# Optimization experiments

Hardware: AMD Instinct MI355X
Metric: run time of the kernel (lower is better)

## Reference

```python
import jax, jax.numpy as jnp
import numpy as np

NUM_EXPERTS = 8
TOP_K = 2
D = 1024


def setup_inputs() -> dict:
    key = jax.random.key(0)
    ks = jax.random.split(key, 5)
    T = 16384
    x = jax.random.normal(ks[0], (T, D), dtype=jnp.float32)
    # torch nn.Linear params: weight [out, in], bias [out]
    Wg = jax.random.normal(ks[1], (NUM_EXPERTS, D), dtype=jnp.float32) * (1.0 / np.sqrt(D))
    bg = jnp.zeros((NUM_EXPERTS,), dtype=jnp.float32)
    We = jax.random.normal(ks[2], (NUM_EXPERTS, D, D), dtype=jnp.float32) * (1.0 / np.sqrt(D))
    be = jax.random.normal(ks[3], (NUM_EXPERTS, D), dtype=jnp.float32) * 0.01
    return {"x": x, "Wg": Wg, "bg": bg, "We": We, "be": be}


def reference(x, Wg, bg, We, be):
    T = x.shape[0]
    # gate logits [T, E]
    gate_logits = x @ Wg.T + bg
    top_k_gates, top_k_idx = jax.lax.top_k(gate_logits, TOP_K)  # [T, K]
    top_k_gates = jax.nn.softmax(top_k_gates, axis=-1)
    # dense per-expert combine weight: sum of gate probs where idx == e
    combine = jnp.zeros((T, NUM_EXPERTS), dtype=x.dtype)
    combine = combine.at[jnp.arange(T)[:, None], top_k_idx].add(top_k_gates)  # [T, E]
    # all-expert dense matmul (faithful to the original naive loop): [E, T, out]
    expert_out = jnp.einsum('td,eod->eto', x, We) + be[:, None, :]
    # weighted combine: output[t] = sum_e combine[t,e] * expert_out[e,t]
    out = jnp.einsum('te,eto->to', combine, expert_out)
    return out
```

## Files before the change

kernel.cpp:

```cpp
#include <hip/hip_runtime.h>
#include <hip/hip_bf16.h>
#include <stdint.h>

#define DDIM 1024
#define NEXP 8
#define SEG  16384

typedef __attribute__((ext_vector_type(8))) short bf16x8;
typedef __attribute__((ext_vector_type(4))) float f32x4;
typedef __attribute__((ext_vector_type(8))) unsigned short u16x8;

__device__ __forceinline__ unsigned short f2bf(float f) {
    union { float f; unsigned int u; } v; v.f = f;
    unsigned int u = v.u;
    return (unsigned short)((u + 0x7FFFu + ((u >> 16) & 1u)) >> 16);
}

__global__ void cvt_we(const float* __restrict__ We, unsigned short* __restrict__ web) {
    size_t idx = ((size_t)blockIdx.x * 256 + threadIdx.x) * 8;
    const float4* p = (const float4*)(We + idx);
    float4 a = p[0], b = p[1];
    u16x8 h;
    h[0] = f2bf(a.x); h[1] = f2bf(a.y); h[2] = f2bf(a.z); h[3] = f2bf(a.w);
    h[4] = f2bf(b.x); h[5] = f2bf(b.y); h[6] = f2bf(b.z); h[7] = f2bf(b.w);
    *(u16x8*)(web + idx) = h;
}

__global__ __launch_bounds__(512) void gate_route(
    const float* __restrict__ x, const float* __restrict__ Wg,
    const float* __restrict__ bg, unsigned short* __restrict__ xb,
    int* __restrict__ cnt, int* __restrict__ tok_list,
    float* __restrict__ gate_list) {

    int wave = threadIdx.x >> 6, lane = threadIdx.x & 63;
    int tbase = blockIdx.x * 32;

    __shared__ int   se[64];
    __shared__ float sg[64];

#pragma unroll
    for (int i = 0; i < 4; i++) {
        int lt = wave * 4 + i;
        int t = tbase + lt;
        const float* xr = x + (size_t)t * DDIM;
        int c0 = lane * 16;

        float4 v[4];
#pragma unroll
        for (int j = 0; j < 4; j++) v[j] = ((const float4*)(xr + c0))[j];

        u16x8 h0, h1;
        h0[0] = f2bf(v[0].x); h0[1] = f2bf(v[0].y); h0[2] = f2bf(v[0].z); h0[3] = f2bf(v[0].w);
        h0[4] = f2bf(v[1].x); h0[5] = f2bf(v[1].y); h0[6] = f2bf(v[1].z); h0[7] = f2bf(v[1].w);
        h1[0] = f2bf(v[2].x); h1[1] = f2bf(v[2].y); h1[2] = f2bf(v[2].z); h1[3] = f2bf(v[2].w);
        h1[4] = f2bf(v[3].x); h1[5] = f2bf(v[3].y); h1[6] = f2bf(v[3].z); h1[7] = f2bf(v[3].w);
        u16x8* xo = (u16x8*)(xb + (size_t)t * DDIM + c0);
        xo[0] = h0; xo[1] = h1;

        float acc[NEXP];
#pragma unroll
        for (int e = 0; e < NEXP; e++) {
            const float4* wg = (const float4*)(Wg + e * DDIM + c0);
            float s = 0.f;
#pragma unroll
            for (int j = 0; j < 4; j++) {
                float4 w = wg[j];
                s += v[j].x * w.x + v[j].y * w.y + v[j].z * w.z + v[j].w * w.w;
            }
            acc[e] = s;
        }
#pragma unroll
        for (int e = 0; e < NEXP; e++) {
#pragma unroll
            for (int o = 32; o > 0; o >>= 1) acc[e] += __shfl_xor(acc[e], o, 64);
        }

        if (lane == 0) {
            float l1 = -1e30f, l2 = -1e30f; int e1 = 0, e2 = 0;
#pragma unroll
            for (int e = 0; e < NEXP; e++) {
                float le = acc[e] + bg[e];
                if (le > l1) { l2 = l1; e2 = e1; l1 = le; e1 = e; }
                else if (le > l2) { l2 = le; e2 = e; }
            }
            float g1 = 1.0f / (1.0f + __expf(l2 - l1));
            float g2 = 1.0f - g1;
            se[lt * 2]     = e1; sg[lt * 2]     = g1;
            se[lt * 2 + 1] = e2; sg[lt * 2 + 1] = g2;
        }
    }
    __syncthreads();

    if (threadIdx.x < NEXP) {
        int e = threadIdx.x;
        int k = 0;
#pragma unroll 8
        for (int i = 0; i < 64; i++) k += (se[i] == e);
        if (k) {
            int p = atomicAdd(cnt + e, k);
            for (int i = 0; i < 64; i++) {
                if (se[i] == e) {
                    tok_list[e * SEG + p]  = (tbase + (i >> 1)) * 2 + (i & 1);
                    gate_list[e * SEG + p] = sg[i];
                    p++;
                }
            }
        }
    }
}

template<bool STORE>
__global__ __launch_bounds__(256, 3) void moe_gemm(
    const unsigned short* __restrict__ xb, const unsigned short* __restrict__ web,
    const float* __restrict__ be, const int* __restrict__ cnt,
    const int* __restrict__ tok_list, const float* __restrict__ gate_list,
    float* __restrict__ dst) {

    int e = blockIdx.y >> 7;
    int m0 = (blockIdx.y & 127) << 7;
    int c = cnt[e];
    if (m0 >= c) return;
    int n0 = blockIdx.x << 7;

    __shared__ unsigned short lA[128 * 64];
    __shared__ unsigned short lB[128 * 64];
    __shared__ int   tok_s[128];
    __shared__ float gate_s[128];

    int tid = threadIdx.x;
    int wave = tid >> 6, lane = tid & 63;

    if (tid < 128) {
        int r = m0 + tid;
        int rc = min(r, c - 1);
        tok_s[tid]  = tok_list[e * SEG + rc];
        gate_s[tid] = (r < c) ? gate_list[e * SEG + rc] : 0.0f;
    }
    __syncthreads();

    int rsub = lane >> 3;
    int gsrc = (lane & 7) ^ rsub;

    const unsigned short* agp[4];
    const unsigned short* bgp[4];
#pragma unroll
    for (int j = 0; j < 4; j++) {
        int row = (wave * 4 + j) * 8 + rsub;
        agp[j] = xb + (size_t)(tok_s[row] >> 1) * DDIM + gsrc * 8;
        bgp[j] = web + ((size_t)e << 20) + (size_t)(n0 + row) * DDIM + gsrc * 8;
    }

    f32x4 acc[4][4];
    f32x4 zz = {0.f, 0.f, 0.f, 0.f};
#pragma unroll
    for (int mi = 0; mi < 4; mi++)
#pragma unroll
        for (int ni = 0; ni < 4; ni++) acc[mi][ni] = zz;

    int wm = (wave >> 1) * 64;
    int wn = (wave & 1) * 64;
    int mrow = lane & 15;
    int q = lane >> 4;

    int offA[4], swA[4], offB[4], swB[4];
#pragma unroll
    for (int i = 0; i < 4; i++) {
        int ra = wm + i * 16 + mrow;
        offA[i] = ra * 64; swA[i] = ra & 7;
        int rb = wn + i * 16 + mrow;
        offB[i] = rb * 64; swB[i] = rb & 7;
    }

    for (int kt = 0; kt < 16; kt++) {
        int k0 = kt * 64;
#pragma unroll
        for (int j = 0; j < 4; j++) {
            __builtin_amdgcn_global_load_lds(
                (const __attribute__((address_space(1))) void*)(agp[j] + k0),
                (__attribute__((address_space(3))) void*)(&lA[(wave * 4 + j) * 512]),
                16, 0, 0);
            __builtin_amdgcn_global_load_lds(
                (const __attribute__((address_space(1))) void*)(bgp[j] + k0),
                (__attribute__((address_space(3))) void*)(&lB[(wave * 4 + j) * 512]),
                16, 0, 0);
        }
        __syncthreads();
#pragma unroll
        for (int kh = 0; kh < 2; kh++) {
            int gq = kh * 4 + q;
            bf16x8 af[4], bfr[4];
#pragma unroll
            for (int i = 0; i < 4; i++)
                af[i] = *(const bf16x8*)&lA[offA[i] + ((gq ^ swA[i]) << 3)];
#pragma unroll
            for (int i = 0; i < 4; i++)
                bfr[i] = *(const bf16x8*)&lB[offB[i] + ((gq ^ swB[i]) << 3)];
#pragma unroll
            for (int mi = 0; mi < 4; mi++)
#pragma unroll
                for (int ni = 0; ni < 4; ni++)
                    acc[mi][ni] = __builtin_amdgcn_mfma_f32_16x16x32_bf16(
                        af[mi], bfr[ni], acc[mi][ni], 0, 0, 0);
        }
        __syncthreads();
    }

#pragma unroll
    for (int ni = 0; ni < 4; ni++) {
        int col = n0 + wn + ni * 16 + mrow;
        float bias = be[e * DDIM + col];
#pragma unroll
        for (int mi = 0; mi < 4; mi++) {
#pragma unroll
            for (int r = 0; r < 4; r++) {
                int rl = wm + mi * 16 + q * 4 + r;
                if (m0 + rl < c) {
                    float g = gate_s[rl];
                    float vv = g * (acc[mi][ni][r] + bias);
                    if (STORE) {
                        dst[(size_t)tok_s[rl] * DDIM + col] = vv;
                    } else {
                        atomicAdd(dst + (size_t)(tok_s[rl] >> 1) * DDIM + col, vv);
                    }
                }
            }
        }
    }
}

__global__ void combine(const float* __restrict__ S, float* __restrict__ out) {
    size_t i = (size_t)blockIdx.x * 256 + threadIdx.x;
    size_t t  = i >> 8;
    size_t c4 = i & 255;
    const float4* r0 = (const float4*)(S + t * 2 * DDIM) + c4;
    const float4* r1 = (const float4*)(S + (t * 2 + 1) * DDIM) + c4;
    float4 a = *r0, b = *r1;
    float4 o = {a.x + b.x, a.y + b.y, a.z + b.z, a.w + b.w};
    ((float4*)out)[i] = o;
}

extern "C" void kernel_launch(void* const* d_in, const int* in_sizes, int n_in,
                              void* d_out, int out_size, void* d_ws, size_t ws_size,
                              hipStream_t stream) {
    const float* x  = (const float*)d_in[0];
    const float* Wg = (const float*)d_in[1];
    const float* bg = (const float*)d_in[2];
    const float* We = (const float*)d_in[3];
    const float* be = (const float*)d_in[4];
    float* out = (float*)d_out;

    char* ws = (char*)d_ws;
    unsigned short* xb  = (unsigned short*)ws;
    unsigned short* web = (unsigned short*)(ws + 33554432);
    int*   tok_list  = (int*)(ws + 33554432 + 16777216);
    float* gate_list = (float*)(ws + 33554432 + 16777216 + 524288);
    int*   cnt       = (int*)(ws + 33554432 + 16777216 + 1048576);
    float* S         = (float*)(ws + 52428800);

    const size_t NEED = 52428800ull + (size_t)32768 * DDIM * 4;

    hipMemsetAsync(cnt, 0, NEXP * sizeof(int), stream);

    cvt_we<<<4096, 256, 0, stream>>>(We, web);
    gate_route<<<512, 512, 0, stream>>>(x, Wg, bg, xb, cnt, tok_list, gate_list);

    if (ws_size >= NEED) {
        moe_gemm<true><<<dim3(8, 1024), 256, 0, stream>>>(xb, web, be, cnt, tok_list, gate_list, S);
        combine<<<16384, 256, 0, stream>>>(S, out);
    } else {
        hipMemsetAsync(d_out, 0, (size_t)out_size * sizeof(float), stream);
        moe_gemm<false><<<dim3(8, 1024), 256, 0, stream>>>(xb, web, be, cnt, tok_list, gate_list, out);
    }
}
```

Measured before the change: 336.6 us.

## Fuse weight conversion into routing kernel, compact GEMM grid, bf16 scratch for combine

Merges the expert-weight bf16 conversion into the gate/route kernel as extra blocks, removing one launch and letting both run concurrently. The GEMM grid is compacted: each block walks the per-expert counts to find its expert and tile, so 264 row tiles replace 1024 mostly-empty ones. The per-slot scratch buffer is stored in bf16 with nontemporal stores and read back by combine at half the traffic. The cost is extra rounding of the partial outputs before summation, which may hurt accuracy.

Measured after the change: 358.6 us. 6.6% more time.

```diff
diff --git a/kernel.cpp b/kernel.cpp
--- a/kernel.cpp
+++ b/kernel.cpp
@@ -15,28 +15,35 @@
     unsigned int u = v.u;
     return (unsigned short)((u + 0x7FFFu + ((u >> 16) & 1u)) >> 16);
 }
-
-__global__ void cvt_we(const float* __restrict__ We, unsigned short* __restrict__ web) {
-    size_t idx = ((size_t)blockIdx.x * 256 + threadIdx.x) * 8;
-    const float4* p = (const float4*)(We + idx);
-    float4 a = p[0], b = p[1];
-    u16x8 h;
-    h[0] = f2bf(a.x); h[1] = f2bf(a.y); h[2] = f2bf(a.z); h[3] = f2bf(a.w);
-    h[4] = f2bf(b.x); h[5] = f2bf(b.y); h[6] = f2bf(b.z); h[7] = f2bf(b.w);
-    *(u16x8*)(web + idx) = h;
-}
-
-__global__ __launch_bounds__(512) void gate_route(
+__device__ __forceinline__ float bf2f(unsigned short h) {
+    union { unsigned int u; float f; } v; v.u = ((unsigned int)h) << 16;
+    return v.f;
+}
+
+__global__ __launch_bounds__(512) void prep(
     const float* __restrict__ x, const float* __restrict__ Wg,
-    const float* __restrict__ bg, unsigned short* __restrict__ xb,
+    const float* __restrict__ bg, const float* __restrict__ We,
+    unsigned short* __restrict__ xb, unsigned short* __restrict__ web,
     int* __restrict__ cnt, int* __restrict__ tok_list,
     float* __restrict__ gate_list) {
 
+    __shared__ int   se[64];
+    __shared__ float sg[64];
+
+    if (blockIdx.x >= 512) {
+        size_t idx = ((size_t)(blockIdx.x - 512) * 512 + threadIdx.x) * 8;
+        const f32x4* p = (const f32x4*)(We + idx);
+        f32x4 a = __builtin_nontemporal_load(p);
+        f32x4 b = __builtin_nontemporal_load(p + 1);
+        u16x8 h;
+        h[0] = f2bf(a[0]); h[1] = f2bf(a[1]); h[2] = f2bf(a[2]); h[3] = f2bf(a[3]);
+        h[4] = f2bf(b[0]); h[5] = f2bf(b[1]); h[6] = f2bf(b[2]); h[7] = f2bf(b[3]);
+        *(u16x8*)(web + idx) = h;
+        return;
+    }
+
     int wave = threadIdx.x >> 6, lane = threadIdx.x & 63;
     int tbase = blockIdx.x * 32;
-
-    __shared__ int   se[64];
-    __shared__ float sg[64];
 
 #pragma unroll
     for (int i = 0; i < 4; i++) {
@@ -114,12 +121,17 @@
     const unsigned short* __restrict__ xb, const unsigned short* __restrict__ web,
     const float* __restrict__ be, const int* __restrict__ cnt,
     const int* __restrict__ tok_list, const float* __restrict__ gate_list,
-    float* __restrict__ dst) {
-
-    int e = blockIdx.y >> 7;
-    int m0 = (blockIdx.y & 127) << 7;
-    int c = cnt[e];
-    if (m0 >= c) return;
+    unsigned short* __restrict__ Sb, float* __restrict__ outa) {
+
+    int id = blockIdx.y, e = 0, c = 0;
+    while (e < NEXP) {
+        c = cnt[e];
+        int mt = (c + 127) >> 7;
+        if (id < mt) break;
+        id -= mt; e++;
+    }
+    if (e == NEXP) return;
+    int m0 = id << 7;
     int n0 = blockIdx.x << 7;
 
     __shared__ unsigned short lA[128 * 64];
@@ -218,9 +230,11 @@
                     float g = gate_s[rl];
                     float vv = g * (acc[mi][ni][r] + bias);
                     if (STORE) {
-                        dst[(size_t)tok_s[rl] * DDIM + col] = vv;
+                        unsigned short hv = f2bf(vv);
+                        __builtin_nontemporal_store(
+                            hv, Sb + (size_t)tok_s[rl] * DDIM + col);
                     } else {
-                        atomicAdd(dst + (size_t)(tok_s[rl] >> 1) * DDIM + col, vv);
+                        atomicAdd(outa + (size_t)(tok_s[rl] >> 1) * DDIM + col, vv);
                     }
                 }
             }
@@ -228,15 +242,22 @@
     }
 }
 
-__global__ void combine(const float* __restrict__ S, float* __restrict__ out) {
+__global__ void combine(const unsigned short* __restrict__ S, float* __restrict__ out) {
     size_t i = (size_t)blockIdx.x * 256 + threadIdx.x;
-    size_t t  = i >> 8;
-    size_t c4 = i & 255;
-    const float4* r0 = (const float4*)(S + t * 2 * DDIM) + c4;
-    const float4* r1 = (const float4*)(S + (t * 2 + 1) * DDIM) + c4;
-    float4 a = *r0, b = *r1;
-    float4 o = {a.x + b.x, a.y + b.y, a.z + b.z, a.w + b.w};
-    ((float4*)out)[i] = o;
+    size_t t = i >> 7;
+    size_t g = i & 127;
+    const u16x8* r0 = (const u16x8*)(S + t * 2 * DDIM) + g;
+    const u16x8* r1 = (const u16x8*)(S + (t * 2 + 1) * DDIM) + g;
+    u16x8 a = __builtin_nontemporal_load(r0);
+    u16x8 b = __builtin_nontemporal_load(r1);
+    f32x4 o0, o1;
+#pragma unroll
+    for (int k = 0; k < 4; k++) o0[k] = bf2f(a[k]) + bf2f(b[k]);
+#pragma unroll
+    for (int k = 0; k < 4; k++) o1[k] = bf2f(a[4 + k]) + bf2f(b[4 + k]);
+    f32x4* op = (f32x4*)(out + t * DDIM + g * 8);
+    __builtin_nontemporal_store(o0, op);
+    __builtin_nontemporal_store(o1, op + 1);
 }
 
 extern "C" void kernel_launch(void* const* d_in, const int* in_sizes, int n_in,
@@ -255,20 +276,21 @@
     int*   tok_list  = (int*)(ws + 33554432 + 16777216);
     float* gate_list = (float*)(ws + 33554432 + 16777216 + 524288);
     int*   cnt       = (int*)(ws + 33554432 + 16777216 + 1048576);
-    float* S         = (float*)(ws + 52428800);
-
-    const size_t NEED = 52428800ull + (size_t)32768 * DDIM * 4;
+    unsigned short* S = (unsigned short*)(ws + 52428800);
+
+    const size_t NEED = 52428800ull + (size_t)32768 * DDIM * 2;
 
     hipMemsetAsync(cnt, 0, NEXP * sizeof(int), stream);
 
-    cvt_we<<<4096, 256, 0, stream>>>(We, web);
-    gate_route<<<512, 512, 0, stream>>>(x, Wg, bg, xb, cnt, tok_list, gate_list);
+    prep<<<2560, 512, 0, stream>>>(x, Wg, bg, We, xb, web, cnt, tok_list, gate_list);
 
     if (ws_size >= NEED) {
-        moe_gemm<true><<<dim3(8, 1024), 256, 0, stream>>>(xb, web, be, cnt, tok_list, gate_list, S);
-        combine<<<16384, 256, 0, stream>>>(S, out);
+        moe_gemm<true><<<dim3(8, 264), 256, 0, stream>>>(
+            xb, web, be, cnt, tok_list, gate_list, S, nullptr);
+        combine<<<8192, 256, 0, stream>>>(S, out);
     } else {
         hipMemsetAsync(d_out, 0, (size_t)out_size * sizeof(float), stream);
-        moe_gemm<false><<<dim3(8, 1024), 256, 0, stream>>>(xb, web, be, cnt, tok_list, gate_list, out);
-    }
-}
+        moe_gemm<false><<<dim3(8, 264), 256, 0, stream>>>(
+            xb, web, be, cnt, tok_list, gate_list, nullptr, out);
+    }
+}
```
